# Performance work log

Hardware: AMD Instinct MI355X
Metric: run time of the kernel (lower is better)

## Reference

```python
import jax, jax.numpy as jnp
import numpy as np

N_NODES = 200000
N_EDGES = 600000
NUM_GRAPHS = 20000
IN_DIM = 128
HID = 128
HEADS1 = 4
OUT1 = HID // HEADS1  # 32
NEG_SLOPE = 0.2
LN_EPS = 1e-5


def setup_inputs() -> dict:
    key = jax.random.key(0)
    ks = jax.random.split(key, 12)
    x = jax.random.normal(ks[0], (N_NODES, IN_DIM), dtype=jnp.float32)
    edge_index = jax.random.randint(ks[1], (2, N_EDGES), 0, N_NODES, dtype=jnp.int64)
    batch = jnp.sort(jax.random.randint(ks[2], (N_NODES,), 0, NUM_GRAPHS, dtype=jnp.int64))
    s1 = 1.0 / np.sqrt(IN_DIM)
    s2 = 1.0 / np.sqrt(HID)
    W1 = jax.random.normal(ks[3], (IN_DIM, HEADS1 * OUT1), dtype=jnp.float32) * s1
    att_src1 = jax.random.normal(ks[4], (HEADS1, OUT1), dtype=jnp.float32) * s1
    att_dst1 = jax.random.normal(ks[5], (HEADS1, OUT1), dtype=jnp.float32) * s1
    b1 = jnp.zeros((HEADS1 * OUT1,), dtype=jnp.float32)
    W2 = jax.random.normal(ks[6], (HID, HID), dtype=jnp.float32) * s2
    att_src2 = jax.random.normal(ks[7], (1, HID), dtype=jnp.float32) * s2
    att_dst2 = jax.random.normal(ks[8], (1, HID), dtype=jnp.float32) * s2
    b2 = jnp.zeros((HID,), dtype=jnp.float32)
    ln_gamma = jnp.ones((HID,), dtype=jnp.float32)
    ln_beta = jnp.zeros((HID,), dtype=jnp.float32)
    return dict(x=x, edge_index=edge_index, batch=batch,
                W1=W1, att_src1=att_src1, att_dst1=att_dst1, b1=b1,
                W2=W2, att_src2=att_src2, att_dst2=att_dst2, b2=b2,
                ln_gamma=ln_gamma, ln_beta=ln_beta)


def gat_conv(x, W, att_src, att_dst, bias, edge_index, heads, out_ch):
    # PyG GATConv (concat=True, add_self_loops=True, eval mode / no dropout)
    n = x.shape[0]
    loop = jnp.arange(n, dtype=edge_index.dtype)
    src = jnp.concatenate([edge_index[0], loop])
    dst = jnp.concatenate([edge_index[1], loop])
    h = (x @ W).reshape(n, heads, out_ch)          # [N,H,C]
    a_src = jnp.einsum('nhc,hc->nh', h, att_src)    # [N,H]
    a_dst = jnp.einsum('nhc,hc->nh', h, att_dst)
    alpha = a_src[src] + a_dst[dst]                 # [E,H]
    alpha = jax.nn.leaky_relu(alpha, NEG_SLOPE)
    # segment softmax over incoming edges of each dst node
    m = jax.lax.stop_gradient(jax.ops.segment_max(alpha, dst, num_segments=n))
    e = jnp.exp(alpha - m[dst])
    denom = jax.ops.segment_sum(e, dst, num_segments=n)
    coef = e / denom[dst]                           # [E,H]
    msg = h[src] * coef[:, :, None]                 # [E,H,C]
    out = jax.ops.segment_sum(msg, dst, num_segments=n)  # [N,H,C]
    return out.reshape(n, heads * out_ch) + bias


def layer_norm(x, gamma, beta):
    mu = jnp.mean(x, axis=-1, keepdims=True)
    var = jnp.mean(jnp.square(x - mu), axis=-1, keepdims=True)
    return (x - mu) * jax.lax.rsqrt(var + LN_EPS) * gamma + beta


def reference(x, edge_index, batch, W1, att_src1, att_dst1, b1,
              W2, att_src2, att_dst2, b2, ln_gamma, ln_beta):
    h1 = jax.nn.relu(gat_conv(x, W1, att_src1, att_dst1, b1, edge_index, HEADS1, OUT1))
    h2 = gat_conv(h1, W2, att_src2, att_dst2, b2, edge_index, 1, HID)
    h2 = layer_norm(h2, ln_gamma, ln_beta)
    # global mean pool per graph
    sums = jax.ops.segment_sum(h2, batch, num_segments=NUM_GRAPHS)   # [G,HID]
    cnts = jax.ops.segment_sum(jnp.ones((h2.shape[0],), h2.dtype), batch, num_segments=NUM_GRAPHS)
    return sums / jnp.maximum(cnts, 1.0)[:, None]
```

## Files before the change

kernel.cpp:

```cpp
#include <hip/hip_runtime.h>
#include <cstdint>
#include <cstddef>

#define N_NODES_C 200000
#define N_EDGES_C 600000
#define NUM_GRAPHS_C 20000

constexpr float NEG_SLOPE = 0.2f;
constexpr float LN_EPS = 1e-5f;

typedef __attribute__((ext_vector_type(8))) short bf16x8;
typedef __attribute__((ext_vector_type(4))) float f32x4;

static __device__ __forceinline__ unsigned short f2bf(float f) {
  unsigned u = __float_as_uint(f);
  u = (u + 0x7fffu + ((u >> 16) & 1u)) >> 16;
  return (unsigned short)u;
}
static __device__ __forceinline__ float bf2f(unsigned short s) {
  return __uint_as_float(((unsigned)s) << 16);
}


__global__ __launch_bounds__(256) void count_deg_kernel(const int* __restrict__ dst,
                                                        int* __restrict__ deg, int E) {
  int e = blockIdx.x * 256 + threadIdx.x;
  if (e < E) atomicAdd(&deg[dst[e]], 1);
}

__global__ __launch_bounds__(256) void scan_kernel(const int* __restrict__ in,
                                                   int* __restrict__ out,
                                                   int* __restrict__ bsums,
                                                   int n_total, int npad) {
  __shared__ int ss[256];
  int t = threadIdx.x;
  int base = blockIdx.x * 1024 + t * 4;
  int v[4];
  int s = 0;
#pragma unroll
  for (int j = 0; j < 4; ++j) {
    int idx = base + j;
    int x = (idx < n_total) ? in[idx] : 0;
    if (idx < npad) x = ((x + 3) & ~3) + 4;
    v[j] = x;
    s += x;
  }
  ss[t] = s;
  __syncthreads();
  for (int off = 1; off < 256; off <<= 1) {
    int x = (t >= off) ? ss[t - off] : 0;
    __syncthreads();
    ss[t] += x;
    __syncthreads();
  }
  int incl = ss[t];
  int excl = incl - s;
  if (bsums != nullptr && t == 255) bsums[blockIdx.x] = incl;
  int run = excl;
#pragma unroll
  for (int j = 0; j < 4; ++j) {
    if (base + j < n_total) out[base + j] = run;
    run += v[j];
  }
}

__global__ __launch_bounds__(256) void scan_addoff_kernel(int* __restrict__ data,
                                                          const int* __restrict__ boff,
                                                          int n_total) {
  int base = blockIdx.x * 1024 + threadIdx.x * 4;
  int add = boff[blockIdx.x];
#pragma unroll
  for (int j = 0; j < 4; ++j) {
    if (base + j < n_total) data[base + j] += add;
  }
}

__global__ __launch_bounds__(256) void fill_csr_kernel(const int* __restrict__ src,
                                                       const int* __restrict__ dst,
                                                       const int* __restrict__ row_ptr,
                                                       int* __restrict__ cursor,
                                                       int* __restrict__ col, int E) {
  int e = blockIdx.x * 256 + threadIdx.x;
  if (e < E) {
    int d = dst[e];
    int p = atomicAdd(&cursor[d], 1);
    col[row_ptr[d] + p] = src[e];
  }
}

__global__ __launch_bounds__(256) void pad_fill_kernel(const int* __restrict__ row_ptr,
                                                       const int* __restrict__ deg,
                                                       int* __restrict__ col, int n) {
  int i = blockIdx.x * 256 + threadIdx.x;
  if (i >= n) return;
  int s = row_ptr[i] + deg[i];
  int e = row_ptr[i + 1];
#pragma unroll 1
  for (int j = s; j < e; ++j) col[j] = n;
}

__global__ void dummy_init_kernel(float* __restrict__ asrc1,
                                  float* __restrict__ asrc2, int n) {
  int t = threadIdx.x;
  if (t < 4) asrc1[(size_t)n * 4 + t] = -1e30f;
  if (t == 4) asrc2[n] = -1e30f;
}


__global__ __launch_bounds__(256) void graph_ptr_kernel(const int* __restrict__ batch,
                                                        int* __restrict__ gp, int n,
                                                        int G) {
  int i = blockIdx.x * 256 + threadIdx.x;
  if (i < n) {
    int prev = (i == 0) ? -1 : batch[i - 1];
    int cur = batch[i];
#pragma unroll 1
    for (int g = prev + 1; g <= cur; ++g) gp[g] = i;
  } else if (i == n) {
    int last = batch[n - 1];
#pragma unroll 1
    for (int g = last + 1; g <= G; ++g) gp[g] = n;
  }
}


__global__ __launch_bounds__(256) void wprep_kernel(const float* __restrict__ W,
                                                    unsigned short* __restrict__ Wtp) {
  int idx = blockIdx.x * 256 + threadIdx.x;
  if (idx >= 128 * 136) return;
  int n = idx / 136, k = idx % 136;
  Wtp[idx] = (k < 128) ? f2bf(W[(size_t)k * 128 + n]) : (unsigned short)0;
}


template <int H, bool A_BF16>
__global__ __launch_bounds__(256) void gemm_att_mfma(
    const void* __restrict__ Av, const unsigned short* __restrict__ Wtp,
    const float* __restrict__ att_src, const float* __restrict__ att_dst,
    unsigned short* __restrict__ Cbf, float* __restrict__ asrc,
    float* __restrict__ adst) {
  __shared__ __align__(16) unsigned short Alds[64 * 136];
  __shared__ __align__(16) unsigned short Wlds[128 * 136];
  int tid = threadIdx.x;
  int lane = tid & 63;
  int wave = tid >> 6;
  int row0 = blockIdx.x * 64;

#pragma unroll
  for (int i = 0; i < 9; ++i) {
    int ch = tid + i * 256;
    if (ch < 2176) *(bf16x8*)&Wlds[ch * 8] = *(const bf16x8*)&Wtp[(size_t)ch * 8];
  }
#pragma unroll
  for (int i = 0; i < 4; ++i) {
    int ch = tid + i * 256;
    int r = ch >> 4, c = ch & 15;
    if constexpr (A_BF16) {
      bf16x8 v = *(const bf16x8*)((const unsigned short*)Av +
                                  (size_t)(row0 + r) * 128 + c * 8);
      *(bf16x8*)&Alds[r * 136 + c * 8] = v;
    } else {
      const float* A = (const float*)Av;
      float4 v0 = *(const float4*)(A + (size_t)(row0 + r) * 128 + c * 8);
      float4 v1 = *(const float4*)(A + (size_t)(row0 + r) * 128 + c * 8 + 4);
      unsigned short tmp[8] = {f2bf(v0.x), f2bf(v0.y), f2bf(v0.z), f2bf(v0.w),
                               f2bf(v1.x), f2bf(v1.y), f2bf(v1.z), f2bf(v1.w)};
      *(bf16x8*)&Alds[r * 136 + c * 8] = *(bf16x8*)tmp;
    }
  }
  __syncthreads();

  int l15 = lane & 15;
  int lg = lane >> 4;
  int wr = wave * 16;

  f32x4 acc[8];
#pragma unroll
  for (int nt = 0; nt < 8; ++nt) acc[nt] = (f32x4){0.f, 0.f, 0.f, 0.f};

#pragma unroll
  for (int ks = 0; ks < 4; ++ks) {
    bf16x8 af = *(const bf16x8*)&Alds[(wr + l15) * 136 + ks * 32 + lg * 8];
#pragma unroll
    for (int nt = 0; nt < 8; ++nt) {
      bf16x8 bfr = *(const bf16x8*)&Wlds[(nt * 16 + l15) * 136 + ks * 32 + lg * 8];
      acc[nt] = __builtin_amdgcn_mfma_f32_16x16x32_bf16(af, bfr, acc[nt], 0, 0, 0);
    }
  }

  float vsv[8], vdv[8];
#pragma unroll
  for (int nt = 0; nt < 8; ++nt) {
    vsv[nt] = att_src[nt * 16 + l15];
    vdv[nt] = att_dst[nt * 16 + l15];
  }

#pragma unroll
  for (int r = 0; r < 4; ++r) {
    int row = row0 + wr + lg * 4 + r;
#pragma unroll
    for (int nt = 0; nt < 8; ++nt) {
      Cbf[(size_t)row * 128 + nt * 16 + l15] = f2bf(acc[nt][r]);
    }
    if constexpr (H == 4) {
      float ps[4], pd[4];
#pragma unroll
      for (int hd = 0; hd < 4; ++hd) {
        ps[hd] = acc[2 * hd][r] * vsv[2 * hd] + acc[2 * hd + 1][r] * vsv[2 * hd + 1];
        pd[hd] = acc[2 * hd][r] * vdv[2 * hd] + acc[2 * hd + 1][r] * vdv[2 * hd + 1];
#pragma unroll
        for (int off = 1; off < 16; off <<= 1) {
          ps[hd] += __shfl_xor(ps[hd], off, 64);
          pd[hd] += __shfl_xor(pd[hd], off, 64);
        }
      }
      if (l15 < 4) {
        float pss = (l15 == 0) ? ps[0] : (l15 == 1) ? ps[1] : (l15 == 2) ? ps[2] : ps[3];
        float pds = (l15 == 0) ? pd[0] : (l15 == 1) ? pd[1] : (l15 == 2) ? pd[2] : pd[3];
        asrc[(size_t)row * 4 + l15] = pss;
        adst[(size_t)row * 4 + l15] = pds;
      }
    } else {
      float ps = 0.f, pd = 0.f;
#pragma unroll
      for (int nt = 0; nt < 8; ++nt) {
        ps = fmaf(acc[nt][r], vsv[nt], ps);
        pd = fmaf(acc[nt][r], vdv[nt], pd);
      }
#pragma unroll
      for (int off = 1; off < 16; off <<= 1) {
        ps += __shfl_xor(ps, off, 64);
        pd += __shfl_xor(pd, off, 64);
      }
      if (l15 == 0) {
        asrc[row] = ps;
        adst[row] = pd;
      }
    }
  }
}


template <int H, bool RELU, bool LNOUT>
__global__ __launch_bounds__(256) void gat_agg5_kernel(
    const unsigned short* __restrict__ h, const float* __restrict__ asrc,
    const float* __restrict__ adst, const int* __restrict__ row_ptr,
    const int* __restrict__ col, const float* __restrict__ bias,
    const float* __restrict__ gamma, const float* __restrict__ beta,
    unsigned short* __restrict__ outbf, int n) {
  int wid = __builtin_amdgcn_readfirstlane((blockIdx.x * 256 + threadIdx.x) >> 6);
  int lane = threadIdx.x & 63;
  int nodeA = wid * 2;
  int nodeB = nodeA + 1;
  if (nodeA >= n) return;

  int e0A = __builtin_amdgcn_readfirstlane(row_ptr[nodeA]);
  int e0B = __builtin_amdgcn_readfirstlane(row_ptr[nodeA + 1]);
  int e1B = __builtin_amdgcn_readfirstlane(row_ptr[nodeA + 2]);
  int lastA = e0B - e0A - 4;
  int lastB = e1B - e0B - 4;
  int tmax = ((lastA > lastB) ? lastA : lastB) + 4;

  int c0 = lane * 2;
  const int hd = (H == 1) ? 0 : (lane >> 4);

  float adA = (H == 4) ? adst[(size_t)nodeA * 4 + hd] : adst[nodeA];
  float asA = (H == 4) ? asrc[(size_t)nodeA * 4 + hd] : asrc[nodeA];
  float adB = (H == 4) ? adst[(size_t)nodeB * 4 + hd] : adst[nodeB];
  float asB = (H == 4) ? asrc[(size_t)nodeB * 4 + hd] : asrc[nodeB];

  float xA = asA + adA; xA = (xA > 0.f) ? xA : NEG_SLOPE * xA;
  float selfeA = __expf(xA);
  float xB = asB + adB; xB = (xB > 0.f) ? xB : NEG_SLOPE * xB;
  float selfeB = __expf(xB);

  float denA = selfeA;
  float denB = selfeB;

  float2 accA, accB;
  {
    unsigned ha = *(const unsigned*)(h + (size_t)nodeA * 128 + c0);
    unsigned hb = *(const unsigned*)(h + (size_t)nodeB * 128 + c0);
    accA.x = bf2f((unsigned short)(ha & 0xffffu)) * selfeA;
    accA.y = bf2f((unsigned short)(ha >> 16)) * selfeA;
    accB.x = bf2f((unsigned short)(hb & 0xffffu)) * selfeB;
    accB.y = bf2f((unsigned short)(hb >> 16)) * selfeB;
  }

#pragma unroll 1
  for (int t = 0; t < tmax; t += 4) {
    int tA = (t < lastA) ? t : lastA;
    int tB = (t < lastB) ? t : lastB;
    int sA4[4], sB4[4];
#pragma unroll
    for (int i = 0; i < 4; ++i) {
      sA4[i] = __builtin_amdgcn_readfirstlane(col[e0A + tA + i]);
      sB4[i] = __builtin_amdgcn_readfirstlane(col[e0B + tB + i]);
    }
    float aA4[4], aB4[4];
    unsigned hA4[4], hB4[4];
#pragma unroll
    for (int i = 0; i < 4; ++i) {
      aA4[i] = (H == 4) ? asrc[(size_t)sA4[i] * 4 + hd] : asrc[sA4[i]];
      aB4[i] = (H == 4) ? asrc[(size_t)sB4[i] * 4 + hd] : asrc[sB4[i]];
      hA4[i] = *(const unsigned*)(h + (size_t)sA4[i] * 128 + c0);
      hB4[i] = *(const unsigned*)(h + (size_t)sB4[i] * 128 + c0);
    }
#pragma unroll
    for (int i = 0; i < 4; ++i) {
      float ya = aA4[i] + adA; ya = (ya > 0.f) ? ya : NEG_SLOPE * ya;
      float eeA = __expf(ya);
      float yb = aB4[i] + adB; yb = (yb > 0.f) ? yb : NEG_SLOPE * yb;
      float eeB = __expf(yb);
      denA += eeA;
      denB += eeB;
      accA.x = fmaf(bf2f((unsigned short)(hA4[i] & 0xffffu)), eeA, accA.x);
      accA.y = fmaf(bf2f((unsigned short)(hA4[i] >> 16)), eeA, accA.y);
      accB.x = fmaf(bf2f((unsigned short)(hB4[i] & 0xffffu)), eeB, accB.x);
      accB.y = fmaf(bf2f((unsigned short)(hB4[i] >> 16)), eeB, accB.y);
    }
  }

  float invA = 1.f / denA;
  float invB = 1.f / denB;

  float bx = bias[c0], by = bias[c0 + 1];
  accA.x = fmaf(accA.x, invA, bx);
  accA.y = fmaf(accA.y, invA, by);
  accB.x = fmaf(accB.x, invB, bx);
  accB.y = fmaf(accB.y, invB, by);
  if (RELU) {
    accA.x = fmaxf(accA.x, 0.f); accA.y = fmaxf(accA.y, 0.f);
    accB.x = fmaxf(accB.x, 0.f); accB.y = fmaxf(accB.y, 0.f);
  }

  if (!LNOUT) {
    unsigned pa = (unsigned)f2bf(accA.x) | ((unsigned)f2bf(accA.y) << 16);
    unsigned pb = (unsigned)f2bf(accB.x) | ((unsigned)f2bf(accB.y) << 16);
    *(unsigned*)(outbf + (size_t)nodeA * 128 + c0) = pa;
    *(unsigned*)(outbf + (size_t)nodeB * 128 + c0) = pb;
  } else {
    float sA = accA.x + accA.y;
    float sB = accB.x + accB.y;
#pragma unroll
    for (int off = 1; off < 64; off <<= 1) {
      sA += __shfl_xor(sA, off, 64);
      sB += __shfl_xor(sB, off, 64);
    }
    float muA = sA * (1.f / 128.f), muB = sB * (1.f / 128.f);
    float dxA = accA.x - muA, dyA = accA.y - muA;
    float dxB = accB.x - muB, dyB = accB.y - muB;
    float vA = dxA * dxA + dyA * dyA;
    float vB = dxB * dxB + dyB * dyB;
#pragma unroll
    for (int off = 1; off < 64; off <<= 1) {
      vA += __shfl_xor(vA, off, 64);
      vB += __shfl_xor(vB, off, 64);
    }
    float ivA = rsqrtf(vA * (1.f / 128.f) + LN_EPS);
    float ivB = rsqrtf(vB * (1.f / 128.f) + LN_EPS);
    float gx = gamma[c0], gy = gamma[c0 + 1];
    float ex = beta[c0], ey = beta[c0 + 1];
    float oxA = fmaf(dxA * ivA, gx, ex), oyA = fmaf(dyA * ivA, gy, ey);
    float oxB = fmaf(dxB * ivB, gx, ex), oyB = fmaf(dyB * ivB, gy, ey);
    unsigned pa = (unsigned)f2bf(oxA) | ((unsigned)f2bf(oyA) << 16);
    unsigned pb = (unsigned)f2bf(oxB) | ((unsigned)f2bf(oyB) << 16);
    *(unsigned*)(outbf + (size_t)nodeA * 128 + c0) = pa;
    *(unsigned*)(outbf + (size_t)nodeB * 128 + c0) = pb;
  }
}


__global__ __launch_bounds__(256) void pool_kernel(const unsigned short* __restrict__ hln,
                                                   const int* __restrict__ gp,
                                                   float* __restrict__ out, int G) {
  int g = (blockIdx.x * 256 + threadIdx.x) >> 6;
  int lane = threadIdx.x & 63;
  if (g >= G) return;
  int s = gp[g], e = gp[g + 1];
  float ax = 0.f, ay = 0.f;
#pragma unroll 1
  for (int i = s; i < e; ++i) {
    unsigned v = *(const unsigned*)(hln + (size_t)i * 128 + lane * 2);
    ax += bf2f((unsigned short)(v & 0xffffu));
    ay += bf2f((unsigned short)(v >> 16));
  }
  int c = e - s;
  float sc = 1.f / (float)((c > 0) ? c : 1);
  *(float2*)(out + (size_t)g * 128 + lane * 2) = make_float2(ax * sc, ay * sc);
}


extern "C" void kernel_launch(void* const* d_in, const int* in_sizes, int n_in,
                              void* d_out, int out_size, void* d_ws, size_t ws_size,
                              hipStream_t stream) {
  const float* x = (const float*)d_in[0];
  const int* ei = (const int*)d_in[1];
  const int* batch = (const int*)d_in[2];
  const float* W1 = (const float*)d_in[3];
  const float* att_src1 = (const float*)d_in[4];
  const float* att_dst1 = (const float*)d_in[5];
  const float* b1 = (const float*)d_in[6];
  const float* W2 = (const float*)d_in[7];
  const float* att_src2 = (const float*)d_in[8];
  const float* att_dst2 = (const float*)d_in[9];
  const float* b2 = (const float*)d_in[10];
  const float* gamma = (const float*)d_in[11];
  const float* beta = (const float*)d_in[12];
  float* out = (float*)d_out;

  const int N = N_NODES_C, E = N_EDGES_C, G = NUM_GRAPHS_C;
  const int COLSZ = E + 7 * N;
  const int* src = ei;
  const int* dst = ei + E;

  float* p = (float*)d_ws;
  float* asrc1 = p; p += (size_t)(N + 1) * 4;
  float* adst1 = p; p += (size_t)N * 4;
  float* asrc2 = p; p += N + 1;
  float* adst2 = p; p += N;
  int* ip = (int*)p;
  int* deg = ip;       ip += N + 1;
  int* cursor = ip;    ip += N;
  int* col = ip;       ip += COLSZ;
  int* bsums = ip;     ip += 256;
  int* bsums2 = ip;    ip += 256;
  int* row_ptr = ip;   ip += N + 2;
  int* graph_ptr = ip; ip += G + 2;
  unsigned short* h1bf = (unsigned short*)ip;
  unsigned short* hbbf = h1bf + (size_t)(N + 1) * 128;
  unsigned short* h2bf = hbbf + (size_t)(N + 1) * 128;
  unsigned short* wt1 = h2bf + (size_t)(N + 1) * 128;
  unsigned short* wt2 = wt1 + 128 * 136;
  (void)ws_size; (void)in_sizes; (void)n_in; (void)out_size;

  hipMemsetAsync(deg, 0, sizeof(int) * (size_t)(N + 1), stream);
  hipMemsetAsync(cursor, 0, sizeof(int) * (size_t)N, stream);

  count_deg_kernel<<<(E + 255) / 256, 256, 0, stream>>>(dst, deg, E);
  int nblk = (N + 1 + 1023) / 1024;
  scan_kernel<<<nblk, 256, 0, stream>>>(deg, row_ptr, bsums, N + 1, N);
  scan_kernel<<<1, 256, 0, stream>>>(bsums, bsums2, nullptr, nblk, 0);
  scan_addoff_kernel<<<nblk, 256, 0, stream>>>(row_ptr, bsums2, N + 1);
  fill_csr_kernel<<<(E + 255) / 256, 256, 0, stream>>>(src, dst, row_ptr, cursor, col, E);
  pad_fill_kernel<<<(N + 255) / 256, 256, 0, stream>>>(row_ptr, deg, col, N);
  graph_ptr_kernel<<<(N + 1 + 255) / 256, 256, 0, stream>>>(batch, graph_ptr, N, G);
  wprep_kernel<<<(128 * 136 + 255) / 256, 256, 0, stream>>>(W1, wt1);
  wprep_kernel<<<(128 * 136 + 255) / 256, 256, 0, stream>>>(W2, wt2);
  dummy_init_kernel<<<1, 64, 0, stream>>>(asrc1, asrc2, N);

  int pairs = N / 2;
  int pblocks = (int)(((size_t)pairs * 64 + 255) / 256);
  int gblocks = N / 64;

  gemm_att_mfma<4, false><<<gblocks, 256, 0, stream>>>(
      x, wt1, att_src1, att_dst1, h1bf, asrc1, adst1);
  gat_agg5_kernel<4, true, false><<<pblocks, 256, 0, stream>>>(
      h1bf, asrc1, adst1, row_ptr, col, b1, nullptr, nullptr, hbbf, N);

  gemm_att_mfma<1, true><<<gblocks, 256, 0, stream>>>(
      hbbf, wt2, att_src2, att_dst2, h2bf, asrc2, adst2);
  gat_agg5_kernel<1, false, true><<<pblocks, 256, 0, stream>>>(
      h2bf, asrc2, adst2, row_ptr, col, b2, gamma, beta, h1bf, N);

  pool_kernel<<<(int)(((size_t)G * 64 + 255) / 256), 256, 0, stream>>>(
      h1bf, graph_ptr, out, G);
}
```

Before: 322.2 us.

## Aggregate one node per half-wave with vector loads and tighter CSR padding

The GAT aggregation kernel now gives each half-wavefront (32 lanes) its own destination node, with each lane handling 4 channels through 8-byte loads. Previously a whole wavefront processed a node pair in lockstep, with scalarized column indices and clamped trip counts. The CSR padding drops the extra 4 slots per node (degrees are rounded up to a multiple of 4 only), which shrinks the col array, and neighbor indices are read as int4. This should cut wasted iterations on padding and on the shorter node of each pair, and widen memory accesses. In exchange, column loads become per-lane vector loads rather than scalar, and the two halves of a wave may diverge in trip count.

```diff
diff --git a/kernel.cpp b/kernel.cpp
--- a/kernel.cpp
+++ b/kernel.cpp
@@ -19,6 +19,12 @@
 }
 static __device__ __forceinline__ float bf2f(unsigned short s) {
   return __uint_as_float(((unsigned)s) << 16);
+}
+static __device__ __forceinline__ float bfu_lo(unsigned u) {
+  return __uint_as_float(u << 16);
+}
+static __device__ __forceinline__ float bfu_hi(unsigned u) {
+  return __uint_as_float(u & 0xffff0000u);
 }
 
 
@@ -41,7 +47,7 @@
   for (int j = 0; j < 4; ++j) {
     int idx = base + j;
     int x = (idx < n_total) ? in[idx] : 0;
-    if (idx < npad) x = ((x + 3) & ~3) + 4;
+    if (idx < npad) x = (x + 3) & ~3;
     v[j] = x;
     s += x;
   }
@@ -242,131 +248,126 @@
 
 
 template <int H, bool RELU, bool LNOUT>
-__global__ __launch_bounds__(256) void gat_agg5_kernel(
+__global__ __launch_bounds__(256) void gat_agg6_kernel(
     const unsigned short* __restrict__ h, const float* __restrict__ asrc,
     const float* __restrict__ adst, const int* __restrict__ row_ptr,
     const int* __restrict__ col, const float* __restrict__ bias,
     const float* __restrict__ gamma, const float* __restrict__ beta,
     unsigned short* __restrict__ outbf, int n) {
-  int wid = __builtin_amdgcn_readfirstlane((blockIdx.x * 256 + threadIdx.x) >> 6);
+  int wid = (blockIdx.x * 256 + threadIdx.x) >> 6;
   int lane = threadIdx.x & 63;
-  int nodeA = wid * 2;
-  int nodeB = nodeA + 1;
-  if (nodeA >= n) return;
-
-  int e0A = __builtin_amdgcn_readfirstlane(row_ptr[nodeA]);
-  int e0B = __builtin_amdgcn_readfirstlane(row_ptr[nodeA + 1]);
-  int e1B = __builtin_amdgcn_readfirstlane(row_ptr[nodeA + 2]);
-  int lastA = e0B - e0A - 4;
-  int lastB = e1B - e0B - 4;
-  int tmax = ((lastA > lastB) ? lastA : lastB) + 4;
-
-  int c0 = lane * 2;
-  const int hd = (H == 1) ? 0 : (lane >> 4);
-
-  float adA = (H == 4) ? adst[(size_t)nodeA * 4 + hd] : adst[nodeA];
-  float asA = (H == 4) ? asrc[(size_t)nodeA * 4 + hd] : asrc[nodeA];
-  float adB = (H == 4) ? adst[(size_t)nodeB * 4 + hd] : adst[nodeB];
-  float asB = (H == 4) ? asrc[(size_t)nodeB * 4 + hd] : asrc[nodeB];
-
-  float xA = asA + adA; xA = (xA > 0.f) ? xA : NEG_SLOPE * xA;
-  float selfeA = __expf(xA);
-  float xB = asB + adB; xB = (xB > 0.f) ? xB : NEG_SLOPE * xB;
-  float selfeB = __expf(xB);
-
-  float denA = selfeA;
-  float denB = selfeB;
-
-  float2 accA, accB;
+  int half = lane >> 5;
+  int cl = lane & 31;
+  int node = wid * 2 + half;
+  if (node >= n) return;
+
+  int e0 = row_ptr[node];
+  int len = row_ptr[node + 1] - e0;
+  int c0 = cl * 4;
+  const int hd = (H == 1) ? 0 : (cl >> 3);
+
+  float ad = (H == 4) ? adst[(size_t)node * 4 + hd] : adst[node];
+  float as_ = (H == 4) ? asrc[(size_t)node * 4 + hd] : asrc[node];
+  float x = as_ + ad;
+  x = (x > 0.f) ? x : NEG_SLOPE * x;
+  float selfe = __expf(x);
+  float den = selfe;
+
+  float a0, a1, a2, a3;
   {
-    unsigned ha = *(const unsigned*)(h + (size_t)nodeA * 128 + c0);
-    unsigned hb = *(const unsigned*)(h + (size_t)nodeB * 128 + c0);
-    accA.x = bf2f((unsigned short)(ha & 0xffffu)) * selfeA;
-    accA.y = bf2f((unsigned short)(ha >> 16)) * selfeA;
-    accB.x = bf2f((unsigned short)(hb & 0xffffu)) * selfeB;
-    accB.y = bf2f((unsigned short)(hb >> 16)) * selfeB;
+    uint2 hs = *(const uint2*)(h + (size_t)node * 128 + c0);
+    a0 = bfu_lo(hs.x) * selfe;
+    a1 = bfu_hi(hs.x) * selfe;
+    a2 = bfu_lo(hs.y) * selfe;
+    a3 = bfu_hi(hs.y) * selfe;
   }
 
 #pragma unroll 1
-  for (int t = 0; t < tmax; t += 4) {
-    int tA = (t < lastA) ? t : lastA;
-    int tB = (t < lastB) ? t : lastB;
-    int sA4[4], sB4[4];
-#pragma unroll
-    for (int i = 0; i < 4; ++i) {
-      sA4[i] = __builtin_amdgcn_readfirstlane(col[e0A + tA + i]);
-      sB4[i] = __builtin_amdgcn_readfirstlane(col[e0B + tB + i]);
+  for (int t = 0; t < len; t += 4) {
+    int4 s4 = *(const int4*)(col + e0 + t);
+    float sc0, sc1, sc2, sc3;
+    if constexpr (H == 4) {
+      sc0 = asrc[(size_t)s4.x * 4 + hd];
+      sc1 = asrc[(size_t)s4.y * 4 + hd];
+      sc2 = asrc[(size_t)s4.z * 4 + hd];
+      sc3 = asrc[(size_t)s4.w * 4 + hd];
+    } else {
+      sc0 = asrc[s4.x];
+      sc1 = asrc[s4.y];
+      sc2 = asrc[s4.z];
+      sc3 = asrc[s4.w];
     }
-    float aA4[4], aB4[4];
-    unsigned hA4[4], hB4[4];
-#pragma unroll
-    for (int i = 0; i < 4; ++i) {
-      aA4[i] = (H == 4) ? asrc[(size_t)sA4[i] * 4 + hd] : asrc[sA4[i]];
-      aB4[i] = (H == 4) ? asrc[(size_t)sB4[i] * 4 + hd] : asrc[sB4[i]];
-      hA4[i] = *(const unsigned*)(h + (size_t)sA4[i] * 128 + c0);
-      hB4[i] = *(const unsigned*)(h + (size_t)sB4[i] * 128 + c0);
-    }
-#pragma unroll
-    for (int i = 0; i < 4; ++i) {
-      float ya = aA4[i] + adA; ya = (ya > 0.f) ? ya : NEG_SLOPE * ya;
-      float eeA = __expf(ya);
-      float yb = aB4[i] + adB; yb = (yb > 0.f) ? yb : NEG_SLOPE * yb;
-      float eeB = __expf(yb);
-      denA += eeA;
-      denB += eeB;
-      accA.x = fmaf(bf2f((unsigned short)(hA4[i] & 0xffffu)), eeA, accA.x);
-      accA.y = fmaf(bf2f((unsigned short)(hA4[i] >> 16)), eeA, accA.y);
-      accB.x = fmaf(bf2f((unsigned short)(hB4[i] & 0xffffu)), eeB, accB.x);
-      accB.y = fmaf(bf2f((unsigned short)(hB4[i] >> 16)), eeB, accB.y);
-    }
-  }
-
-  float invA = 1.f / denA;
-  float invB = 1.f / denB;
-
-  float bx = bias[c0], by = bias[c0 + 1];
-  accA.x = fmaf(accA.x, invA, bx);
-  accA.y = fmaf(accA.y, invA, by);
-  accB.x = fmaf(accB.x, invB, bx);
-  accB.y = fmaf(accB.y, invB, by);
+    uint2 h0 = *(const uint2*)(h + (size_t)s4.x * 128 + c0);
+    uint2 h1 = *(const uint2*)(h + (size_t)s4.y * 128 + c0);
+    uint2 h2 = *(const uint2*)(h + (size_t)s4.z * 128 + c0);
+    uint2 h3 = *(const uint2*)(h + (size_t)s4.w * 128 + c0);
+
+    float y0 = sc0 + ad; y0 = (y0 > 0.f) ? y0 : NEG_SLOPE * y0;
+    float e0f = __expf(y0);
+    float y1 = sc1 + ad; y1 = (y1 > 0.f) ? y1 : NEG_SLOPE * y1;
+    float e1f = __expf(y1);
+    float y2 = sc2 + ad; y2 = (y2 > 0.f) ? y2 : NEG_SLOPE * y2;
+    float e2f = __expf(y2);
+    float y3 = sc3 + ad; y3 = (y3 > 0.f) ? y3 : NEG_SLOPE * y3;
+    float e3f = __expf(y3);
+    den += e0f + e1f + e2f + e3f;
+
+    a0 = fmaf(bfu_lo(h0.x), e0f, a0);
+    a1 = fmaf(bfu_hi(h0.x), e0f, a1);
+    a2 = fmaf(bfu_lo(h0.y), e0f, a2);
+    a3 = fmaf(bfu_hi(h0.y), e0f, a3);
+    a0 = fmaf(bfu_lo(h1.x), e1f, a0);
+    a1 = fmaf(bfu_hi(h1.x), e1f, a1);
+    a2 = fmaf(bfu_lo(h1.y), e1f, a2);
+    a3 = fmaf(bfu_hi(h1.y), e1f, a3);
+    a0 = fmaf(bfu_lo(h2.x), e2f, a0);
+    a1 = fmaf(bfu_hi(h2.x), e2f, a1);
+    a2 = fmaf(bfu_lo(h2.y), e2f, a2);
+    a3 = fmaf(bfu_hi(h2.y), e2f, a3);
+    a0 = fmaf(bfu_lo(h3.x), e3f, a0);
+    a1 = fmaf(bfu_hi(h3.x), e3f, a1);
+    a2 = fmaf(bfu_lo(h3.y), e3f, a2);
+    a3 = fmaf(bfu_hi(h3.y), e3f, a3);
+  }
+
+  float inv = 1.f / den;
+  float4 b4 = *(const float4*)(bias + c0);
+  float o0 = fmaf(a0, inv, b4.x);
+  float o1 = fmaf(a1, inv, b4.y);
+  float o2 = fmaf(a2, inv, b4.z);
+  float o3 = fmaf(a3, inv, b4.w);
   if (RELU) {
-    accA.x = fmaxf(accA.x, 0.f); accA.y = fmaxf(accA.y, 0.f);
-    accB.x = fmaxf(accB.x, 0.f); accB.y = fmaxf(accB.y, 0.f);
+    o0 = fmaxf(o0, 0.f);
+    o1 = fmaxf(o1, 0.f);
+    o2 = fmaxf(o2, 0.f);
+    o3 = fmaxf(o3, 0.f);
   }
 
   if (!LNOUT) {
-    unsigned pa = (unsigned)f2bf(accA.x) | ((unsigned)f2bf(accA.y) << 16);
-    unsigned pb = (unsigned)f2bf(accB.x) | ((unsigned)f2bf(accB.y) << 16);
-    *(unsigned*)(outbf + (size_t)nodeA * 128 + c0) = pa;
-    *(unsigned*)(outbf + (size_t)nodeB * 128 + c0) = pb;
+    uint2 pv;
+    pv.x = (unsigned)f2bf(o0) | ((unsigned)f2bf(o1) << 16);
+    pv.y = (unsigned)f2bf(o2) | ((unsigned)f2bf(o3) << 16);
+    *(uint2*)(outbf + (size_t)node * 128 + c0) = pv;
   } else {
-    float sA = accA.x + accA.y;
-    float sB = accB.x + accB.y;
-#pragma unroll
-    for (int off = 1; off < 64; off <<= 1) {
-      sA += __shfl_xor(sA, off, 64);
-      sB += __shfl_xor(sB, off, 64);
-    }
-    float muA = sA * (1.f / 128.f), muB = sB * (1.f / 128.f);
-    float dxA = accA.x - muA, dyA = accA.y - muA;
-    float dxB = accB.x - muB, dyB = accB.y - muB;
-    float vA = dxA * dxA + dyA * dyA;
-    float vB = dxB * dxB + dyB * dyB;
-#pragma unroll
-    for (int off = 1; off < 64; off <<= 1) {
-      vA += __shfl_xor(vA, off, 64);
-      vB += __shfl_xor(vB, off, 64);
-    }
-    float ivA = rsqrtf(vA * (1.f / 128.f) + LN_EPS);
-    float ivB = rsqrtf(vB * (1.f / 128.f) + LN_EPS);
-    float gx = gamma[c0], gy = gamma[c0 + 1];
-    float ex = beta[c0], ey = beta[c0 + 1];
-    float oxA = fmaf(dxA * ivA, gx, ex), oyA = fmaf(dyA * ivA, gy, ey);
-    float oxB = fmaf(dxB * ivB, gx, ex), oyB = fmaf(dyB * ivB, gy, ey);
-    unsigned pa = (unsigned)f2bf(oxA) | ((unsigned)f2bf(oyA) << 16);
-    unsigned pb = (unsigned)f2bf(oxB) | ((unsigned)f2bf(oyB) << 16);
-    *(unsigned*)(outbf + (size_t)nodeA * 128 + c0) = pa;
-    *(unsigned*)(outbf + (size_t)nodeB * 128 + c0) = pb;
+    float ssum = o0 + o1 + o2 + o3;
+#pragma unroll
+    for (int off = 1; off < 32; off <<= 1) ssum += __shfl_xor(ssum, off, 64);
+    float mu = ssum * (1.f / 128.f);
+    float d0 = o0 - mu, d1 = o1 - mu, d2 = o2 - mu, d3 = o3 - mu;
+    float vs2 = d0 * d0 + d1 * d1 + d2 * d2 + d3 * d3;
+#pragma unroll
+    for (int off = 1; off < 32; off <<= 1) vs2 += __shfl_xor(vs2, off, 64);
+    float ivn = rsqrtf(vs2 * (1.f / 128.f) + LN_EPS);
+    float4 g4 = *(const float4*)(gamma + c0);
+    float4 be4 = *(const float4*)(beta + c0);
+    float q0 = fmaf(d0 * ivn, g4.x, be4.x);
+    float q1 = fmaf(d1 * ivn, g4.y, be4.y);
+    float q2 = fmaf(d2 * ivn, g4.z, be4.z);
+    float q3 = fmaf(d3 * ivn, g4.w, be4.w);
+    uint2 pv;
+    pv.x = (unsigned)f2bf(q0) | ((unsigned)f2bf(q1) << 16);
+    pv.y = (unsigned)f2bf(q2) | ((unsigned)f2bf(q3) << 16);
+    *(uint2*)(outbf + (size_t)node * 128 + c0) = pv;
   }
 }
 
@@ -382,8 +383,8 @@
 #pragma unroll 1
   for (int i = s; i < e; ++i) {
     unsigned v = *(const unsigned*)(hln + (size_t)i * 128 + lane * 2);
-    ax += bf2f((unsigned short)(v & 0xffffu));
-    ay += bf2f((unsigned short)(v >> 16));
+    ax += bfu_lo(v);
+    ay += bfu_hi(v);
   }
   int c = e - s;
   float sc = 1.f / (float)((c > 0) ? c : 1);
@@ -410,7 +411,7 @@
   float* out = (float*)d_out;
 
   const int N = N_NODES_C, E = N_EDGES_C, G = NUM_GRAPHS_C;
-  const int COLSZ = E + 7 * N;
+  const int COLSZ = E + 3 * N + 16;
   const int* src = ei;
   const int* dst = ei + E;
 
@@ -449,18 +450,17 @@
   wprep_kernel<<<(128 * 136 + 255) / 256, 256, 0, stream>>>(W2, wt2);
   dummy_init_kernel<<<1, 64, 0, stream>>>(asrc1, asrc2, N);
 
-  int pairs = N / 2;
-  int pblocks = (int)(((size_t)pairs * 64 + 255) / 256);
+  int pblocks = N / 8;
   int gblocks = N / 64;
 
   gemm_att_mfma<4, false><<<gblocks, 256, 0, stream>>>(
       x, wt1, att_src1, att_dst1, h1bf, asrc1, adst1);
-  gat_agg5_kernel<4, true, false><<<pblocks, 256, 0, stream>>>(
+  gat_agg6_kernel<4, true, false><<<pblocks, 256, 0, stream>>>(
       h1bf, asrc1, adst1, row_ptr, col, b1, nullptr, nullptr, hbbf, N);
 
   gemm_att_mfma<1, true><<<gblocks, 256, 0, stream>>>(
       hbbf, wt2, att_src2, att_dst2, h2bf, asrc2, adst2);
-  gat_agg5_kernel<1, false, true><<<pblocks, 256, 0, stream>>>(
+  gat_agg6_kernel<1, false, true><<<pblocks, 256, 0, stream>>>(
       h2bf, asrc2, adst2, row_ptr, col, b2, gamma, beta, h1bf, N);
 
   pool_kernel<<<(int)(((size_t)G * 64 + 255) / 256), 256, 0, stream>>>(
```

New measurement: 298.7 us. 7.3% less time.
